# Kernel tuning notes

Hardware: AMD Instinct MI355X
Metric: run time of the kernel (lower is better)

The kernel has to match this reference:

```python
import jax, jax.numpy as jnp
import numpy as np

N_EMBD = 384
N_HEAD = 6
HEAD_SIZE = N_EMBD // N_HEAD
D_FF = 4 * N_EMBD
LN_EPS = 1e-3  # keras LayerNormalization default epsilon


def setup_inputs() -> dict:
    key = jax.random.key(0)
    ks = jax.random.split(key, 12)
    B, T = 4, 2048
    s = 1.0 / np.sqrt(N_EMBD)
    return {
        "x": jax.random.normal(ks[0], (B, T, N_EMBD), dtype=jnp.float32),
        "Wq": jax.random.normal(ks[1], (N_EMBD, N_EMBD), dtype=jnp.float32) * s,
        "Wk": jax.random.normal(ks[2], (N_EMBD, N_EMBD), dtype=jnp.float32) * s,
        "Wv": jax.random.normal(ks[3], (N_EMBD, N_EMBD), dtype=jnp.float32) * s,
        "Wo": jax.random.normal(ks[4], (N_EMBD, N_EMBD), dtype=jnp.float32) * s,
        "bo": jnp.zeros((N_EMBD,), dtype=jnp.float32),
        "W1": jax.random.normal(ks[5], (N_EMBD, D_FF), dtype=jnp.float32) * s,
        "b1": jnp.zeros((D_FF,), dtype=jnp.float32),
        "W2": jax.random.normal(ks[6], (D_FF, N_EMBD), dtype=jnp.float32) * (1.0 / np.sqrt(D_FF)),
        "b2": jnp.zeros((N_EMBD,), dtype=jnp.float32),
        "g1": jnp.ones((N_EMBD,), dtype=jnp.float32),
        "be1": jnp.zeros((N_EMBD,), dtype=jnp.float32),
        "g2": jnp.ones((N_EMBD,), dtype=jnp.float32),
        "be2": jnp.zeros((N_EMBD,), dtype=jnp.float32),
    }


def _layer_norm(x, gamma, beta):
    mu = jnp.mean(x, axis=-1, keepdims=True)
    var = jnp.mean(jnp.square(x - mu), axis=-1, keepdims=True)
    return (x - mu) * jax.lax.rsqrt(var + LN_EPS) * gamma + beta


def _block(x, Wq, Wk, Wv, Wo, bo, W1, b1, W2, b2, g1, be1, g2, be2):
    B, T, C = x.shape
    H, D = N_HEAD, HEAD_SIZE
    q = (x @ Wq).reshape(B, T, H, D).transpose(0, 2, 1, 3)  # [B,H,T,D]
    k = (x @ Wk).reshape(B, T, H, D).transpose(0, 2, 1, 3)
    v = (x @ Wv).reshape(B, T, H, D).transpose(0, 2, 1, 3)
    scores = jnp.einsum("bhqd,bhkd->bhqk", q, k) / jnp.sqrt(jnp.float32(D))
    causal = jnp.tril(jnp.ones((T, T), dtype=bool))
    scores = jnp.where(causal, scores, jnp.float32(-1e9))
    attn = jax.nn.softmax(scores, axis=-1)  # dropout is identity at inference
    out = jnp.einsum("bhqk,bhkd->bhqd", attn, v)
    out = out.transpose(0, 2, 1, 3).reshape(B, T, H * D)
    y = out @ Wo + bo
    x = _layer_norm(x + y, g1, be1)
    y = jax.nn.relu(x @ W1 + b1) @ W2 + b2
    return _layer_norm(x + y, g2, be2)


def reference(x, Wq, Wk, Wv, Wo, bo, W1, b1, W2, b2, g1, be1, g2, be2):
    return _block(x, Wq, Wk, Wv, Wo, bo, W1, b1, W2, b2, g1, be1, g2, be2)
```

## Files before the change

kernel.cpp:

```cpp
#include <hip/hip_runtime.h>

#define C_DIM  384
#define HEADS  6
#define HD     64
#define FF_DIM 1536
#define LN_EPS 1e-3f
#define TSEQ   2048
#define BATCH  4
#define LOG2E  1.4426950408889634f
#define QK_SCALE 0.18033688011112042f

typedef __attribute__((ext_vector_type(4))) float          f32x4;
typedef __attribute__((ext_vector_type(4))) float          float4_t;
typedef __attribute__((ext_vector_type(8))) short          bfrag;
typedef __attribute__((ext_vector_type(4))) unsigned short ushort4_t;
typedef __attribute__((ext_vector_type(8))) unsigned short ushort8_t;

__device__ inline unsigned short f2bf(float f) {
    unsigned int u = __builtin_bit_cast(unsigned int, f);
    u += 0x7fff + ((u >> 16) & 1);
    return (unsigned short)(u >> 16);
}
__device__ inline unsigned short f2bf_t(float f) {
    return (unsigned short)(__builtin_bit_cast(unsigned int, f) >> 16);
}
__device__ inline float bf2f(unsigned short u) {
    return __builtin_bit_cast(float, (unsigned int)u << 16);
}

__device__ inline void gload_lds16(const void* g, void* l) {
    __builtin_amdgcn_global_load_lds(
        (const __attribute__((address_space(1))) unsigned int*)g,
        (__attribute__((address_space(3))) unsigned int*)l,
        16, 0, 0);
}

__global__ __launch_bounds__(256)
void transpose_all(const float* __restrict__ Wq, const float* __restrict__ Wk,
                   const float* __restrict__ Wv, const float* __restrict__ Wo,
                   const float* __restrict__ W1, const float* __restrict__ W2,
                   unsigned short* __restrict__ Dqkv, unsigned short* __restrict__ Do_,
                   unsigned short* __restrict__ D1, unsigned short* __restrict__ D2)
{
    __shared__ float tile[32][33];
    const int bidx = blockIdx.x;
    const float* W; unsigned short* D;
    int K, N, nx, ny;
    if (bidx < 576) {
        const int z = bidx / 144, r = bidx % 144;
        W = z == 0 ? Wq : (z == 1 ? Wk : (z == 2 ? Wv : Wo));
        D = z == 3 ? Do_ : Dqkv + (size_t)z * C_DIM * C_DIM;
        K = N = C_DIM; nx = r % 12; ny = r / 12;
    } else if (bidx < 1152) {
        const int r = bidx - 576;
        W = W1; D = D1; K = C_DIM; N = FF_DIM; nx = r % 48; ny = r / 48;
    } else {
        const int r = bidx - 1152;
        W = W2; D = D2; K = FF_DIM; N = C_DIM; nx = r % 12; ny = r / 12;
    }
    const int tx = threadIdx.x, ty = threadIdx.y;
    const int n0 = nx * 32, k0 = ny * 32;
    #pragma unroll
    for (int i = 0; i < 32; i += 8)
        tile[ty + i][tx] = W[(size_t)(k0 + ty + i) * N + n0 + tx];
    __syncthreads();
    #pragma unroll
    for (int i = 0; i < 32; i += 8)
        D[(size_t)(n0 + ty + i) * K + k0 + tx] = f2bf(tile[tx][ty + i]);
}

__global__ __launch_bounds__(256)
void cvt_f32_bf16_x4(const float* __restrict__ in, unsigned short* __restrict__ out, int n4)
{
    int i = blockIdx.x * 256 + threadIdx.x;
    if (i >= n4) return;
    float4_t v = ((const float4_t*)in)[i];
    ushort4_t o = { f2bf(v.x), f2bf(v.y), f2bf(v.z), f2bf(v.w) };
    ((ushort4_t*)out)[i] = o;
}

__global__ __launch_bounds__(256)
void vtrans_kernel(const unsigned short* __restrict__ qkv,
                   unsigned short* __restrict__ vt)
{
    __shared__ unsigned short tile[32][34];
    const int tx = threadIdx.x, ty = threadIdx.y;
    const int bh = blockIdx.z, b = bh / HEADS, h = bh % HEADS;
    const int t0 = blockIdx.x * 32, d0 = blockIdx.y * 32;
    #pragma unroll
    for (int i = 0; i < 32; i += 8)
        tile[ty + i][tx] = qkv[(size_t)(b * TSEQ + t0 + ty + i) * 1152 + 2 * C_DIM + h * HD + d0 + tx];
    __syncthreads();
    #pragma unroll
    for (int i = 0; i < 32; i += 8)
        vt[((size_t)bh * HD + d0 + ty + i) * TSEQ + t0 + tx] = tile[tx][ty + i];
}

template<int OBF16, int BIAS, int RELU, int QSCALE, int KSPLIT>
__global__ __launch_bounds__(256)
void gemm_lds(const unsigned short* __restrict__ A, const unsigned short* __restrict__ Bt,
              const float* __restrict__ bias, void* __restrict__ Cv,
              unsigned short* __restrict__ ktc,
              int M, int N, int K)
{
    __shared__ __align__(16) unsigned short As[16 * 512];
    __shared__ __align__(16) unsigned short Bs[16 * 512];

    const int t = threadIdx.x, lane = t & 63, w = t >> 6;
    const int ln16 = lane & 15, hi16 = lane >> 4;
    const int wr = w >> 1, wc = w & 1;
    const int row0 = blockIdx.y * 128, col0 = blockIdx.x * 128;

    f32x4 acc[4][4] = {};

    for (int k0 = 0; k0 < K; k0 += 64) {
        #pragma unroll
        for (int i = 0; i < 4; ++i) {
            const int f  = w * 4 + i;
            const int ks = f >> 3, rf = f & 7;
            const int row = rf * 16 + ln16;
            const int kc  = k0 + ks * 32 + hi16 * 8;
            gload_lds16(&A [(size_t)(row0 + row) * K + kc], &As[f * 512]);
            gload_lds16(&Bt[(size_t)(col0 + row) * K + kc], &Bs[f * 512]);
        }
        __syncthreads();
        #pragma unroll
        for (int ks = 0; ks < 2; ++ks) {
            bfrag a[4], b[4];
            #pragma unroll
            for (int i = 0; i < 4; ++i)
                a[i] = *(const bfrag*)&As[(ks * 8 + wr * 4 + i) * 512 + lane * 8];
            #pragma unroll
            for (int j = 0; j < 4; ++j)
                b[j] = *(const bfrag*)&Bs[(ks * 8 + wc * 4 + j) * 512 + lane * 8];
            #pragma unroll
            for (int i = 0; i < 4; ++i)
                #pragma unroll
                for (int j = 0; j < 4; ++j)
                    acc[i][j] = __builtin_amdgcn_mfma_f32_16x16x32_bf16(a[i], b[j], acc[i][j], 0, 0, 0);
        }
        __syncthreads();
    }

    #pragma unroll
    for (int j = 0; j < 4; ++j) {
        const int cbase = col0 + wc * 64 + j * 16;
        const int col = cbase + ln16;
        const float bv = BIAS ? bias[col] : 0.0f;
        const float sc = (QSCALE && col < C_DIM) ? QK_SCALE : 1.0f;
        const bool kdest = KSPLIT && (cbase >= C_DIM) && (cbase < 2 * C_DIM);
        #pragma unroll
        for (int i = 0; i < 4; ++i) {
            #pragma unroll
            for (int e = 0; e < 4; ++e) {
                const int row = row0 + wr * 64 + i * 16 + hi16 * 4 + e;
                float v = acc[i][j][e] + bv;
                if (RELU) v = fmaxf(v, 0.0f);
                if (QSCALE) v *= sc;
                if (kdest) {
                    const int b  = row >> 11, tt = row & 2047;
                    const int hd = col - C_DIM;
                    const int bh = b * HEADS + (hd >> 6);
                    ktc[((size_t)bh * TSEQ + tt) * HD + (hd & 63)] = f2bf(v);
                } else if (OBF16) {
                    ((unsigned short*)Cv)[(size_t)row * N + col] = f2bf(v);
                } else {
                    ((float*)Cv)[(size_t)row * N + col] = v;
                }
            }
        }
    }
}

template<int OBF16, int BIAS, int RELU>
__global__ __launch_bounds__(256)
void gemm_lds64(const unsigned short* __restrict__ A, const unsigned short* __restrict__ Bt,
                const float* __restrict__ bias, void* __restrict__ Cv,
                int M, int N, int K)
{
    __shared__ __align__(16) unsigned short As[8 * 512];
    __shared__ __align__(16) unsigned short Bs[16 * 512];

    const int t = threadIdx.x, lane = t & 63, w = t >> 6;
    const int ln16 = lane & 15, hi16 = lane >> 4;
    const int wr = w >> 1, wc = w & 1;
    const int row0 = blockIdx.y * 64, col0 = blockIdx.x * 128;

    f32x4 acc[2][4] = {};

    for (int k0 = 0; k0 < K; k0 += 64) {
        #pragma unroll
        for (int i = 0; i < 2; ++i) {
            const int f  = w * 2 + i;
            const int ks = f >> 2, rf = f & 3;
            gload_lds16(&A[(size_t)(row0 + rf * 16 + ln16) * K + k0 + ks * 32 + hi16 * 8],
                        &As[f * 512]);
        }
        #pragma unroll
        for (int i = 0; i < 4; ++i) {
            const int f  = w * 4 + i;
            const int ks = f >> 3, cf = f & 7;
            gload_lds16(&Bt[(size_t)(col0 + cf * 16 + ln16) * K + k0 + ks * 32 + hi16 * 8],
                        &Bs[f * 512]);
        }
        __syncthreads();
        #pragma unroll
        for (int ks = 0; ks < 2; ++ks) {
            bfrag a[2], b[4];
            #pragma unroll
            for (int i = 0; i < 2; ++i)
                a[i] = *(const bfrag*)&As[(ks * 4 + wr * 2 + i) * 512 + lane * 8];
            #pragma unroll
            for (int j = 0; j < 4; ++j)
                b[j] = *(const bfrag*)&Bs[(ks * 8 + wc * 4 + j) * 512 + lane * 8];
            #pragma unroll
            for (int i = 0; i < 2; ++i)
                #pragma unroll
                for (int j = 0; j < 4; ++j)
                    acc[i][j] = __builtin_amdgcn_mfma_f32_16x16x32_bf16(a[i], b[j], acc[i][j], 0, 0, 0);
        }
        __syncthreads();
    }

    #pragma unroll
    for (int j = 0; j < 4; ++j) {
        const int col = col0 + wc * 64 + j * 16 + ln16;
        const float bv = BIAS ? bias[col] : 0.0f;
        #pragma unroll
        for (int i = 0; i < 2; ++i) {
            #pragma unroll
            for (int e = 0; e < 4; ++e) {
                const int row = row0 + wr * 32 + i * 16 + hi16 * 4 + e;
                float v = acc[i][j][e] + bv;
                if (RELU) v = fmaxf(v, 0.0f);
                if (OBF16) ((unsigned short*)Cv)[(size_t)row * N + col] = f2bf(v);
                else       ((float*)Cv)[(size_t)row * N + col] = v;
            }
        }
    }
}

__device__ inline void qk16(const bfrag (&qf)[2][2], const bfrag (&kf)[4][2],
                            f32x4 (&sf)[2][4])
{
    __builtin_amdgcn_s_setprio(1);
    #pragma unroll
    for (int jt = 0; jt < 4; ++jt)
        #pragma unroll
        for (int ks = 0; ks < 2; ++ks) {
            sf[0][jt] = __builtin_amdgcn_mfma_f32_16x16x32_bf16(qf[0][ks], kf[jt][ks], sf[0][jt], 0, 0, 0);
            sf[1][jt] = __builtin_amdgcn_mfma_f32_16x16x32_bf16(qf[1][ks], kf[jt][ks], sf[1][jt], 0, 0, 0);
        }
    __builtin_amdgcn_s_setprio(0);
}

__device__ inline void softmax_pv(f32x4 (&sf)[2][4], const bfrag (&vf)[4][2],
                                  f32x4 (&acc)[2][4],
                                  float (&mrow)[2][4], float (&lrow)[2][4],
                                  unsigned short (*Ps)[72],
                                  int tok0, int kt, bool last, int ln16, int hi16)
{
    float lmax[2][4];
    bool need = false;
    #pragma unroll
    for (int rf = 0; rf < 2; ++rf)
        #pragma unroll
        for (int e = 0; e < 4; ++e) {
            const int row = tok0 + rf * 16 + hi16 * 4 + e;
            float mx = -1e30f;
            #pragma unroll
            for (int jt = 0; jt < 4; ++jt) {
                float sv = sf[rf][jt][e];
                if (last && (kt * 64 + jt * 16 + ln16 > row)) sv = -1e30f;
                mx = fmaxf(mx, sv);
            }
            lmax[rf][e] = mx;
            need = need || (mx > mrow[rf][e] + 8.0f);
        }
    if (__any(need)) {
        #pragma unroll
        for (int rf = 0; rf < 2; ++rf)
            #pragma unroll
            for (int e = 0; e < 4; ++e) {
                float rm = lmax[rf][e];
                rm = fmaxf(rm, __shfl_xor(rm, 1));
                rm = fmaxf(rm, __shfl_xor(rm, 2));
                rm = fmaxf(rm, __shfl_xor(rm, 4));
                rm = fmaxf(rm, __shfl_xor(rm, 8));
                const float mn = fmaxf(mrow[rf][e], rm);
                const float corr = exp2f(mrow[rf][e] - mn);
                mrow[rf][e] = mn;
                lrow[rf][e] *= corr;
                #pragma unroll
                for (int dt = 0; dt < 4; ++dt) acc[rf][dt][e] *= corr;
            }
    }

    #pragma unroll
    for (int rf = 0; rf < 2; ++rf)
        #pragma unroll
        for (int jt = 0; jt < 4; ++jt)
            #pragma unroll
            for (int e = 0; e < 4; ++e) {
                const int row = tok0 + rf * 16 + hi16 * 4 + e;
                float sv = sf[rf][jt][e];
                if (last && (kt * 64 + jt * 16 + ln16 > row)) sv = -1e30f;
                const float pe = exp2f(sv - mrow[rf][e]);
                lrow[rf][e] += pe;
                Ps[rf * 16 + hi16 * 4 + e][jt * 16 + ln16] = f2bf_t(pe);
            }

    bfrag pf[2][2];
    #pragma unroll
    for (int rf = 0; rf < 2; ++rf)
        #pragma unroll
        for (int ks = 0; ks < 2; ++ks)
            pf[rf][ks] = *(const bfrag*)&Ps[rf * 16 + ln16][ks * 32 + hi16 * 8];
    __builtin_amdgcn_s_setprio(1);
    #pragma unroll
    for (int ks = 0; ks < 2; ++ks)
        #pragma unroll
        for (int rf = 0; rf < 2; ++rf)
            #pragma unroll
            for (int dt = 0; dt < 4; ++dt)
                acc[rf][dt] = __builtin_amdgcn_mfma_f32_16x16x32_bf16(pf[rf][ks], vf[dt][ks], acc[rf][dt], 0, 0, 0);
    __builtin_amdgcn_s_setprio(0);
}

__global__ __launch_bounds__(64)
void attn_kernel(const unsigned short* __restrict__ qkv,
                 const unsigned short* __restrict__ ktc,
                 const unsigned short* __restrict__ vt,
                 unsigned short* __restrict__ att,
                 unsigned short* __restrict__ pacc,
                 float* __restrict__ pml)
{
    __shared__ __align__(16) unsigned short Ps[32][72];
    const int lane = threadIdx.x;
    const int ln16 = lane & 15, hi16 = lane >> 4;
    const int bid = blockIdx.x;
    const int xcd = bid & 7;
    const int i   = bid >> 3;
    int bh, qw, kt0, kte, ck = 0;
    bool heavy;
    if (i < 192) {
        qw = 63 - (i / 6);
        const int r = i % 6;
        bh = xcd * 3 + (r >> 1);
        ck = r & 1;
        const int NT = (qw >> 1) + 1;
        const int half = NT >> 1;
        kt0 = ck ? half : 0;
        kte = ck ? NT : half;
        heavy = true;
    } else {
        const int j = i - 192;
        qw = 31 - (j / 3);
        bh = xcd * 3 + (j % 3);
        kt0 = 0;
        kte = (qw >> 1) + 1;
        heavy = false;
    }
    const int NTfull = (qw >> 1) + 1;
    const int b = bh / HEADS, h = bh % HEADS;
    const int tok0 = qw * 32;
    const size_t qrow0 = (size_t)b * TSEQ;

    bfrag qf[2][2];
    #pragma unroll
    for (int rf = 0; rf < 2; ++rf)
        #pragma unroll
        for (int ks = 0; ks < 2; ++ks)
            qf[rf][ks] = *(const bfrag*)&qkv[(qrow0 + tok0 + rf * 16 + ln16) * 1152 + h * HD + ks * 32 + hi16 * 8];

    f32x4 acc[2][4] = {};
    float mrow[2][4], lrow[2][4];
    #pragma unroll
    for (int rf = 0; rf < 2; ++rf)
        #pragma unroll
        for (int e = 0; e < 4; ++e) { mrow[rf][e] = -1e30f; lrow[rf][e] = 0.0f; }

    const unsigned short* Kb = ktc + (size_t)bh * TSEQ * HD;
    const unsigned short* Vb = vt  + (size_t)bh * HD * TSEQ;

    bfrag kf[4][2];
    #pragma unroll
    for (int jt = 0; jt < 4; ++jt)
        #pragma unroll
        for (int ks = 0; ks < 2; ++ks)
            kf[jt][ks] = *(const bfrag*)&Kb[(size_t)(kt0 * 64 + jt * 16 + ln16) * HD + ks * 32 + hi16 * 8];

    for (int kt = kt0; kt < kte; ++kt) {
        bfrag vf[4][2];
        #pragma unroll
        for (int dt = 0; dt < 4; ++dt)
            #pragma unroll
            for (int ks = 0; ks < 2; ++ks)
                vf[dt][ks] = *(const bfrag*)&Vb[(size_t)(dt * 16 + ln16) * TSEQ + kt * 64 + ks * 32 + hi16 * 8];

        f32x4 sf[2][4] = {};
        qk16(qf, kf, sf);

        if (kt + 1 < kte) {
            #pragma unroll
            for (int jt = 0; jt < 4; ++jt)
                #pragma unroll
                for (int ks = 0; ks < 2; ++ks)
                    kf[jt][ks] = *(const bfrag*)&Kb[(size_t)((kt + 1) * 64 + jt * 16 + ln16) * HD + ks * 32 + hi16 * 8];
        }

        softmax_pv(sf, vf, acc, mrow, lrow, Ps, tok0, kt, kt == NTfull - 1, ln16, hi16);
    }

    float lsum[2][4];
    #pragma unroll
    for (int rf = 0; rf < 2; ++rf)
        #pragma unroll
        for (int e = 0; e < 4; ++e) {
            float l = lrow[rf][e];
            l += __shfl_xor(l, 1);
            l += __shfl_xor(l, 2);
            l += __shfl_xor(l, 4);
            l += __shfl_xor(l, 8);
            lsum[rf][e] = l;
        }

    if (!heavy) {
        #pragma unroll
        for (int rf = 0; rf < 2; ++rf)
            #pragma unroll
            for (int e = 0; e < 4; ++e) {
                const float inv = 1.0f / lsum[rf][e];
                const size_t row = qrow0 + tok0 + rf * 16 + hi16 * 4 + e;
                #pragma unroll
                for (int dt = 0; dt < 4; ++dt)
                    att[row * C_DIM + h * HD + dt * 16 + ln16] = f2bf(acc[rf][dt][e] * inv);
            }
    } else {
        const int sidx = bh * 32 + (qw - 32);
        const size_t pb = (size_t)sidx * 2 + ck;
        #pragma unroll
        for (int rf = 0; rf < 2; ++rf)
            #pragma unroll
            for (int dt = 0; dt < 4; ++dt)
                #pragma unroll
                for (int e = 0; e < 4; ++e) {
                    const int row = rf * 16 + hi16 * 4 + e;
                    pacc[(pb * 32 + row) * 64 + dt * 16 + ln16] = f2bf(acc[rf][dt][e]);
                }
        if (ln16 == 0) {
            #pragma unroll
            for (int rf = 0; rf < 2; ++rf)
                #pragma unroll
                for (int e = 0; e < 4; ++e) {
                    const int row = rf * 16 + hi16 * 4 + e;
                    pml[pb * 64 + row * 2 + 0] = mrow[rf][e];
                    pml[pb * 64 + row * 2 + 1] = lsum[rf][e];
                }
        }
    }
}

__global__ __launch_bounds__(256)
void attn_combine(const unsigned short* __restrict__ pacc,
                  const float* __restrict__ pml,
                  unsigned short* __restrict__ att)
{
    const int sidx = blockIdx.x;
    const int bh = sidx >> 5;
    const int qw = 32 + (sidx & 31);
    const int b = bh / HEADS, h = bh % HEADS;
    const int tid = threadIdx.x;
    const int row = tid >> 3;
    const int d0  = (tid & 7) * 8;

    const float m0 = pml[((size_t)sidx * 2 + 0) * 64 + row * 2 + 0];
    const float l0 = pml[((size_t)sidx * 2 + 0) * 64 + row * 2 + 1];
    const float m1 = pml[((size_t)sidx * 2 + 1) * 64 + row * 2 + 0];
    const float l1 = pml[((size_t)sidx * 2 + 1) * 64 + row * 2 + 1];
    const float M  = fmaxf(m0, m1);
    const float w0 = exp2f(m0 - M), w1 = exp2f(m1 - M);
    const float invL = 1.0f / (l0 * w0 + l1 * w1);

    ushort8_t a0 = *(const ushort8_t*)&pacc[(((size_t)sidx * 2 + 0) * 32 + row) * 64 + d0];
    ushort8_t a1 = *(const ushort8_t*)&pacc[(((size_t)sidx * 2 + 1) * 32 + row) * 64 + d0];
    ushort8_t rv;
    #pragma unroll
    for (int k = 0; k < 8; ++k) {
        const float v0 = bf2f(a0[k]);
        const float v1 = bf2f(a1[k]);
        rv[k] = f2bf((v0 * w0 + v1 * w1) * invL);
    }
    const size_t grow = (size_t)b * TSEQ + qw * 32 + row;
    *(ushort8_t*)&att[grow * C_DIM + h * HD + d0] = rv;
}

template<int ABF16, int WF32, int WBF>
__global__ __launch_bounds__(256)
void ln_residual_kernel(const void* __restrict__ Av, const float* __restrict__ R,
                        const float* __restrict__ gamma, const float* __restrict__ beta,
                        float* __restrict__ out, unsigned short* __restrict__ outb, int Mrows)
{
    const int lane = threadIdx.x & 63;
    const int wv   = threadIdx.x >> 6;
    const int row  = blockIdx.x * 4 + wv;
    if (row >= Mrows) return;
    const size_t off = (size_t)row * C_DIM;

    float v[6];
    float sum = 0.0f;
    #pragma unroll
    for (int j = 0; j < 6; ++j) {
        const int c = lane + 64 * j;
        const float a = ABF16 ? bf2f(((const unsigned short*)Av)[off + c])
                              : ((const float*)Av)[off + c];
        v[j] = a + R[off + c];
        sum += v[j];
    }
    #pragma unroll
    for (int o = 1; o < 64; o <<= 1) sum += __shfl_xor(sum, o);
    const float mu = sum * (1.0f / C_DIM);

    float sq = 0.0f;
    #pragma unroll
    for (int j = 0; j < 6; ++j) { const float d = v[j] - mu; sq = fmaf(d, d, sq); }
    #pragma unroll
    for (int o = 1; o < 64; o <<= 1) sq += __shfl_xor(sq, o);
    const float rstd = rsqrtf(sq * (1.0f / C_DIM) + LN_EPS);

    #pragma unroll
    for (int j = 0; j < 6; ++j) {
        const int c = lane + 64 * j;
        const float r = (v[j] - mu) * rstd * gamma[c] + beta[c];
        if (WF32) out[off + c] = r;
        if (WBF)  outb[off + c] = f2bf(r);
    }
}

extern "C" void kernel_launch(void* const* d_in, const int* in_sizes, int n_in,
                              void* d_out, int out_size, void* d_ws, size_t ws_size,
                              hipStream_t stream)
{
    const float* x   = (const float*)d_in[0];
    const float* Wq  = (const float*)d_in[1];
    const float* Wk  = (const float*)d_in[2];
    const float* Wv  = (const float*)d_in[3];
    const float* Wo  = (const float*)d_in[4];
    const float* bo  = (const float*)d_in[5];
    const float* W1  = (const float*)d_in[6];
    const float* b1  = (const float*)d_in[7];
    const float* W2  = (const float*)d_in[8];
    const float* b2  = (const float*)d_in[9];
    const float* g1  = (const float*)d_in[10];
    const float* be1 = (const float*)d_in[11];
    const float* g2  = (const float*)d_in[12];
    const float* be2 = (const float*)d_in[13];
    float* out = (float*)d_out;

    const int M = BATCH * TSEQ;
    const size_t MC = (size_t)M * C_DIM;

    char* ws = (char*)d_ws;
    unsigned short* qkv = (unsigned short*)ws;
    unsigned short* vt  = (unsigned short*)(ws + (size_t)M*1152*2);
    unsigned short* att = (unsigned short*)(ws + (size_t)M*1152*2 + (size_t)BATCH*HEADS*HD*TSEQ*2);
    unsigned short* h1  = (unsigned short*)ws;
    char* p2 = ws + (size_t)M*1152*2 + (size_t)BATCH*HEADS*HD*TSEQ*2 + MC*2;
    unsigned short* xb  = (unsigned short*)p2;
    float* y   = (float*)(p2 + MC*2);
    unsigned short* ktc = (unsigned short*)(p2 + MC*2 + MC*4);
    unsigned short* x1b = (unsigned short*)(p2 + MC*2 + 2*MC*4);
    char* p3 = p2 + MC*2 + 2*MC*4 + MC*2;
    unsigned short* Wqkv_t = (unsigned short*)p3;
    unsigned short* Wo_t   = Wqkv_t + (size_t)3*C_DIM*C_DIM;
    unsigned short* W1_t   = Wo_t   + (size_t)C_DIM*C_DIM;
    unsigned short* W2_t   = W1_t   + (size_t)FF_DIM*C_DIM;

    unsigned short* pacc = (unsigned short*)(p2 + MC*2);
    float* pml = (float*)(p2 + MC*2 + (size_t)1536*32*64*2);

    dim3 b256(256), b328(32, 8);

    transpose_all<<<dim3(1728), b328, 0, stream>>>(
        Wq, Wk, Wv, Wo, W1, W2, Wqkv_t, Wo_t, W1_t, W2_t);

    cvt_f32_bf16_x4<<<dim3((MC/4 + 255)/256), b256, 0, stream>>>(x, xb, (int)(MC/4));

    gemm_lds<1, 0, 0, 1, 1><<<dim3(3*C_DIM/128, M/128), b256, 0, stream>>>(
        xb, Wqkv_t, nullptr, qkv, ktc, M, 3*C_DIM, C_DIM);

    vtrans_kernel<<<dim3(TSEQ/32, HD/32, BATCH*HEADS), b328, 0, stream>>>(qkv, vt);

    attn_kernel<<<dim3(2304), dim3(64), 0, stream>>>(qkv, ktc, vt, att, pacc, pml);
    attn_combine<<<dim3(768), b256, 0, stream>>>(pacc, pml, att);

    gemm_lds64<0, 1, 0><<<dim3(C_DIM/128, M/64), b256, 0, stream>>>(
        att, Wo_t, bo, y, M, C_DIM, C_DIM);

    ln_residual_kernel<0, 0, 1><<<dim3(M/4), b256, 0, stream>>>(
        x, y, g1, be1, nullptr, x1b, M);

    gemm_lds<1, 1, 1, 0, 0><<<dim3(FF_DIM/128, M/128), b256, 0, stream>>>(
        x1b, W1_t, b1, h1, nullptr, M, FF_DIM, C_DIM);

    gemm_lds64<0, 1, 0><<<dim3(C_DIM/128, M/64), b256, 0, stream>>>(
        h1, W2_t, b2, y, M, C_DIM, FF_DIM);

    ln_residual_kernel<1, 1, 0><<<dim3(M/4), b256, 0, stream>>>(
        x1b, y, g2, be2, out, nullptr, M);
}
```

Before: 195.4 us.

## Merge weight transpose with input cast, add XCD-aware GEMM tile mapping, vectorize LayerNorm

Folds the fp32-to-bf16 conversion of x into the weight transpose kernel as extra blocks, removing one launch. Remaps GEMM workgroup indices so consecutive tiles are grouped onto the same XCD, aiming for better L2 reuse of the A and B operands. Vectorizes the LayerNorm loads and stores to two elements per lane. The remap assumes the grid size is a multiple of 8, and the LayerNorm change alters the per-lane access pattern.

```diff
diff --git a/kernel.cpp b/kernel.cpp
--- a/kernel.cpp
+++ b/kernel.cpp
@@ -10,6 +10,7 @@
 #define LOG2E  1.4426950408889634f
 #define QK_SCALE 0.18033688011112042f
 
+typedef __attribute__((ext_vector_type(2))) float          f32x2;
 typedef __attribute__((ext_vector_type(4))) float          f32x4;
 typedef __attribute__((ext_vector_type(4))) float          float4_t;
 typedef __attribute__((ext_vector_type(8))) short          bfrag;
@@ -35,15 +36,29 @@
         16, 0, 0);
 }
 
+__device__ inline int xcd_chunk(int flat, int nwg) {
+    return (flat >> 3) + (flat & 7) * (nwg >> 3);
+}
+
 __global__ __launch_bounds__(256)
-void transpose_all(const float* __restrict__ Wq, const float* __restrict__ Wk,
-                   const float* __restrict__ Wv, const float* __restrict__ Wo,
-                   const float* __restrict__ W1, const float* __restrict__ W2,
-                   unsigned short* __restrict__ Dqkv, unsigned short* __restrict__ Do_,
-                   unsigned short* __restrict__ D1, unsigned short* __restrict__ D2)
+void prep_all(const float* __restrict__ Wq, const float* __restrict__ Wk,
+              const float* __restrict__ Wv, const float* __restrict__ Wo,
+              const float* __restrict__ W1, const float* __restrict__ W2,
+              const float* __restrict__ x,
+              unsigned short* __restrict__ Dqkv, unsigned short* __restrict__ Do_,
+              unsigned short* __restrict__ D1, unsigned short* __restrict__ D2,
+              unsigned short* __restrict__ xb)
 {
     __shared__ float tile[32][33];
     const int bidx = blockIdx.x;
+    const int tx = threadIdx.x, ty = threadIdx.y;
+    if (bidx >= 1728) {
+        const int i = (bidx - 1728) * 256 + ty * 32 + tx;
+        float4_t v = ((const float4_t*)x)[i];
+        ushort4_t o = { f2bf(v.x), f2bf(v.y), f2bf(v.z), f2bf(v.w) };
+        ((ushort4_t*)xb)[i] = o;
+        return;
+    }
     const float* W; unsigned short* D;
     int K, N, nx, ny;
     if (bidx < 576) {
@@ -58,7 +73,6 @@
         const int r = bidx - 1152;
         W = W2; D = D2; K = FF_DIM; N = C_DIM; nx = r % 12; ny = r / 12;
     }
-    const int tx = threadIdx.x, ty = threadIdx.y;
     const int n0 = nx * 32, k0 = ny * 32;
     #pragma unroll
     for (int i = 0; i < 32; i += 8)
@@ -67,16 +81,6 @@
     #pragma unroll
     for (int i = 0; i < 32; i += 8)
         D[(size_t)(n0 + ty + i) * K + k0 + tx] = f2bf(tile[tx][ty + i]);
-}
-
-__global__ __launch_bounds__(256)
-void cvt_f32_bf16_x4(const float* __restrict__ in, unsigned short* __restrict__ out, int n4)
-{
-    int i = blockIdx.x * 256 + threadIdx.x;
-    if (i >= n4) return;
-    float4_t v = ((const float4_t*)in)[i];
-    ushort4_t o = { f2bf(v.x), f2bf(v.y), f2bf(v.z), f2bf(v.w) };
-    ((ushort4_t*)out)[i] = o;
 }
 
 __global__ __launch_bounds__(256)
@@ -109,7 +113,9 @@
     const int t = threadIdx.x, lane = t & 63, w = t >> 6;
     const int ln16 = lane & 15, hi16 = lane >> 4;
     const int wr = w >> 1, wc = w & 1;
-    const int row0 = blockIdx.y * 128, col0 = blockIdx.x * 128;
+    const int nwg = gridDim.x * gridDim.y;
+    const int L = xcd_chunk(blockIdx.y * gridDim.x + blockIdx.x, nwg);
+    const int row0 = (L / gridDim.x) * 128, col0 = (L % gridDim.x) * 128;
 
     f32x4 acc[4][4] = {};
 
@@ -184,7 +190,9 @@
     const int t = threadIdx.x, lane = t & 63, w = t >> 6;
     const int ln16 = lane & 15, hi16 = lane >> 4;
     const int wr = w >> 1, wc = w & 1;
-    const int row0 = blockIdx.y * 64, col0 = blockIdx.x * 128;
+    const int nwg = gridDim.x * gridDim.y;
+    const int L = xcd_chunk(blockIdx.y * gridDim.x + blockIdx.x, nwg);
+    const int row0 = (L / gridDim.x) * 64, col0 = (L % gridDim.x) * 128;
 
     f32x4 acc[2][4] = {};
 
@@ -510,12 +518,21 @@
     float v[6];
     float sum = 0.0f;
     #pragma unroll
-    for (int j = 0; j < 6; ++j) {
-        const int c = lane + 64 * j;
-        const float a = ABF16 ? bf2f(((const unsigned short*)Av)[off + c])
-                              : ((const float*)Av)[off + c];
-        v[j] = a + R[off + c];
-        sum += v[j];
+    for (int j = 0; j < 3; ++j) {
+        const int c = lane * 2 + 128 * j;
+        float a0, a1;
+        if (ABF16) {
+            const unsigned int u = *(const unsigned int*)&((const unsigned short*)Av)[off + c];
+            a0 = bf2f((unsigned short)(u & 0xffff));
+            a1 = bf2f((unsigned short)(u >> 16));
+        } else {
+            f32x2 a = *(const f32x2*)&((const float*)Av)[off + c];
+            a0 = a.x; a1 = a.y;
+        }
+        f32x2 r = *(const f32x2*)&R[off + c];
+        v[2 * j]     = a0 + r.x;
+        v[2 * j + 1] = a1 + r.y;
+        sum += v[2 * j] + v[2 * j + 1];
     }
     #pragma unroll
     for (int o = 1; o < 64; o <<= 1) sum += __shfl_xor(sum, o);
@@ -529,11 +546,17 @@
     const float rstd = rsqrtf(sq * (1.0f / C_DIM) + LN_EPS);
 
     #pragma unroll
-    for (int j = 0; j < 6; ++j) {
-        const int c = lane + 64 * j;
-        const float r = (v[j] - mu) * rstd * gamma[c] + beta[c];
-        if (WF32) out[off + c] = r;
-        if (WBF)  outb[off + c] = f2bf(r);
+    for (int j = 0; j < 3; ++j) {
+        const int c = lane * 2 + 128 * j;
+        f32x2 g  = *(const f32x2*)&gamma[c];
+        f32x2 be = *(const f32x2*)&beta[c];
+        const float r0 = (v[2 * j]     - mu) * rstd * g.x + be.x;
+        const float r1 = (v[2 * j + 1] - mu) * rstd * g.y + be.y;
+        if (WF32) { f32x2 o = { r0, r1 }; *(f32x2*)&out[off + c] = o; }
+        if (WBF) {
+            const unsigned int o = (unsigned int)f2bf(r0) | ((unsigned int)f2bf(r1) << 16);
+            *(unsigned int*)&outb[off + c] = o;
+        }
     }
 }
 
@@ -581,10 +604,8 @@
 
     dim3 b256(256), b328(32, 8);
 
-    transpose_all<<<dim3(1728), b328, 0, stream>>>(
-        Wq, Wk, Wv, Wo, W1, W2, Wqkv_t, Wo_t, W1_t, W2_t);
-
-    cvt_f32_bf16_x4<<<dim3((MC/4 + 255)/256), b256, 0, stream>>>(x, xb, (int)(MC/4));
+    prep_all<<<dim3(1728 + 3072), b328, 0, stream>>>(
+        Wq, Wk, Wv, Wo, W1, W2, x, Wqkv_t, Wo_t, W1_t, W2_t, xb);
 
     gemm_lds<1, 0, 0, 1, 1><<<dim3(3*C_DIM/128, M/128), b256, 0, stream>>>(
         xb, Wqkv_t, nullptr, qkv, ktc, M, 3*C_DIM, C_DIM);
```

Measured after the change: 192.8 us. No clear change (-1.3%).
